# Optimization experiments

Measured on AMD Instinct MI355X. Metric: run time of the kernel, lower is better.

Reference implementation:

```python
import jax, jax.numpy as jnp
import numpy as np

EMB = 1024
HEADS = 16

def setup_inputs() -> dict:
    key = jax.random.key(0)
    ks = jax.random.split(key, 9)
    s = 1.0 / np.sqrt(EMB)
    x = jax.random.normal(ks[0], (2, 2048, EMB), dtype=jnp.float32)
    Wq = jax.random.normal(ks[1], (EMB, EMB), dtype=jnp.float32) * s
    bq = jax.random.normal(ks[2], (EMB,), dtype=jnp.float32) * s
    Wk = jax.random.normal(ks[3], (EMB, EMB), dtype=jnp.float32) * s
    bk = jax.random.normal(ks[4], (EMB,), dtype=jnp.float32) * s
    Wv = jax.random.normal(ks[5], (EMB, EMB), dtype=jnp.float32) * s
    bv = jax.random.normal(ks[6], (EMB,), dtype=jnp.float32) * s
    Wo = jax.random.normal(ks[7], (EMB, EMB), dtype=jnp.float32) * s
    bo = jax.random.normal(ks[8], (EMB,), dtype=jnp.float32) * s
    return {"x": x, "Wq": Wq, "bq": bq, "Wk": Wk, "bk": bk, "Wv": Wv, "bv": bv, "Wo": Wo, "bo": bo}

def reference(x, Wq, bq, Wk, bk, Wv, bv, Wo, bo):
    B, N, E = x.shape
    H = HEADS
    D = E // H
    # q/k/v projections, split heads: b n (h d) -> b h n d
    def proj(W, b):
        y = jnp.einsum('bne,ef->bnf', x, W.T) + b
        return y.reshape(B, N, H, D).transpose(0, 2, 1, 3)
    q = proj(Wq, bq)
    k = proj(Wk, bk)
    v = proj(Wv, bv)
    energy = jnp.einsum('bhqd,bhkd->bhqk', q, k)
    scaling = jnp.asarray(E, x.dtype) ** 0.5  # note: sqrt(emb_size), as in source
    att = jax.nn.softmax(energy / scaling, axis=-1)
    out = jnp.einsum('bhqk,bhkd->bhqd', att, v)
    out = out.transpose(0, 2, 1, 3).reshape(B, N, E)  # b h n d -> b n (h d)
    return jnp.einsum('bne,ef->bnf', out, Wo.T) + bo
```

## Files before the change

### kernel.cpp

```cpp
#include <hip/hip_runtime.h>
#include <hip/hip_bf16.h>
#include <stdint.h>

typedef __bf16 bf16;
typedef __bf16 bf16x8 __attribute__((ext_vector_type(8)));
typedef __bf16 bf16x4 __attribute__((ext_vector_type(4)));
typedef __bf16 bf16x2 __attribute__((ext_vector_type(2)));
typedef float  f32x4  __attribute__((ext_vector_type(4)));
typedef float  f32x16 __attribute__((ext_vector_type(16)));
typedef unsigned int uint;

#define MFMA(a,b,c)   __builtin_amdgcn_mfma_f32_16x16x32_bf16((a),(b),(c),0,0,0)
#define MFMA32(a,b,c) __builtin_amdgcn_mfma_f32_32x32x16_bf16((a),(b),(c),0,0,0)
#define EXP2(x)       __builtin_amdgcn_exp2f(x)

__device__ __forceinline__ void gload_lds16(const void* g, void* lds) {
  __builtin_amdgcn_global_load_lds(
      (const __attribute__((address_space(1))) uint32_t*)g,
      (__attribute__((address_space(3))) uint32_t*)lds, 16, 0, 0);
}

__device__ __forceinline__ uint pk_bf16(float lo, float hi) {
  bf16x2 v; v[0] = (bf16)lo; v[1] = (bf16)hi;
  return __builtin_bit_cast(uint, v);
}

__global__ __launch_bounds__(256) void k_cvt(
    const float* __restrict__ x,
    const float* __restrict__ wq, const float* __restrict__ wk,
    const float* __restrict__ wv, const float* __restrict__ wo,
    bf16* __restrict__ xb, bf16* __restrict__ wqb, bf16* __restrict__ wkb,
    bf16* __restrict__ wvb, bf16* __restrict__ wob)
{
  int r = blockIdx.y;
  const float* s; bf16* d; int n;
  switch (r) {
    case 0: s = x;  d = xb;  n = 4194304; break;
    case 1: s = wq; d = wqb; n = 1048576; break;
    case 2: s = wk; d = wkb; n = 1048576; break;
    case 3: s = wv; d = wvb; n = 1048576; break;
    default: s = wo; d = wob; n = 1048576; break;
  }
  int i = (blockIdx.x * 256 + threadIdx.x) * 8;
  if (i >= n) return;
  const float4* sp = (const float4*)(s + i);
  float4 a = sp[0], b = sp[1];
  bf16x8 o;
  o[0]=(bf16)a.x; o[1]=(bf16)a.y; o[2]=(bf16)a.z; o[3]=(bf16)a.w;
  o[4]=(bf16)b.x; o[5]=(bf16)b.y; o[6]=(bf16)b.z; o[7]=(bf16)b.w;
  *(bf16x8*)(d + i) = o;
}

__global__ __launch_bounds__(256, 2) void k_gemm_qkv(
    const bf16* __restrict__ A,
    const bf16* __restrict__ Wq, const bf16* __restrict__ Wk, const bf16* __restrict__ Wv,
    const float* __restrict__ bq, const float* __restrict__ bk, const float* __restrict__ bv,
    bf16* __restrict__ Qw, bf16* __restrict__ Kw, bf16* __restrict__ Vtw)
{
  __shared__ __align__(16) char As[2][8192];
  __shared__ __align__(16) char Bs[2][8192];
  int tid = threadIdx.x;
  int wv4 = tid >> 6, l = tid & 63, lo = l & 15, hi = l >> 4;
  int f = blockIdx.y * 32 + blockIdx.x;
  int xcd = f & 7, i8 = f >> 3;
  int mt = xcd * 4 + (i8 & 3);
  int ft = i8 >> 2;
  int wsel = ft >> 3;
  const bf16* W = (wsel == 0) ? Wq : (wsel == 1) ? Wk : Wv;
  const float* bias = (wsel == 0) ? bq : (wsel == 1) ? bk : bv;
  int f0 = (ft & 7) * 128;
  const bf16* Ab = A + (size_t)mt * 128 * 1024;
  const bf16* Wb = W + (size_t)f0 * 1024;
  const bf16* Pa = (wsel < 2) ? Wb : Ab;
  const bf16* Pb = (wsel < 2) ? Ab : Wb;
  int wm = wv4 >> 1, wf = wv4 & 1;
  f32x4 acc[4][4];
  #pragma unroll
  for (int i = 0; i < 4; i++)
    #pragma unroll
    for (int j = 0; j < 4; j++) acc[i][j] = (f32x4){0.f, 0.f, 0.f, 0.f};

  #define STAGEG(t, bi) {                                              \
    int k0 = (t) * 32;                                                 \
    _Pragma("unroll")                                                  \
    for (int p = 0; p < 2; p++) {                                      \
      int sp = p * 256 + tid;                                          \
      int row = sp >> 2, s = sp & 3;                                   \
      int gc = k0 + 8 * (s ^ ((row >> 1) & 3));                        \
      gload_lds16(Pa + (size_t)row * 1024 + gc, As[bi] + sp * 16);     \
      gload_lds16(Pb + (size_t)row * 1024 + gc, Bs[bi] + sp * 16);     \
    } }

  STAGEG(0, 0);
  for (int t = 0; t < 32; ++t) {
    __syncthreads();
    if (t < 31) STAGEG(t + 1, (t + 1) & 1);
    const char* Ac = As[t & 1];
    const char* Bc = Bs[t & 1];
    bf16x8 af[4], bfr[4];
    #pragma unroll
    for (int ms = 0; ms < 4; ms++) {
      int row = wm * 64 + ms * 16 + lo;
      af[ms] = *(const bf16x8*)(Ac + row * 64 + 16 * (hi ^ ((row >> 1) & 3)));
    }
    #pragma unroll
    for (int fs = 0; fs < 4; fs++) {
      int row = wf * 64 + fs * 16 + lo;
      bfr[fs] = *(const bf16x8*)(Bc + row * 64 + 16 * (hi ^ ((row >> 1) & 3)));
    }
    __builtin_amdgcn_s_setprio(1);
    #pragma unroll
    for (int ms = 0; ms < 4; ms++)
      #pragma unroll
      for (int fs = 0; fs < 4; fs++)
        acc[ms][fs] = MFMA(af[ms], bfr[fs], acc[ms][fs]);
    __builtin_amdgcn_s_setprio(0);
  }
  #undef STAGEG

  if (wsel < 2) {
    bf16* Outp = (wsel == 0) ? Qw : Kw;
    float qs = (wsel == 0) ? 0.0450842199527801f : 1.0f;
    #pragma unroll
    for (int ms = 0; ms < 4; ms++) {
      int fl = f0 + wm * 64 + ms * 16 + hi * 4;
      int h = fl >> 6, dd = fl & 63;
      float4 b4 = *(const float4*)(bias + fl);
      #pragma unroll
      for (int fs = 0; fs < 4; fs++) {
        int m = mt * 128 + wf * 64 + fs * 16 + lo;
        int b = m >> 11, nn = m & 2047;
        bf16x4 w;
        #pragma unroll
        for (int r = 0; r < 4; r++)
          w[r] = (bf16)((acc[ms][fs][r] + ((const float*)&b4)[r]) * qs);
        *(bf16x4*)(Outp + (((size_t)(b * 16 + h) * 2048 + nn) * 64) + dd) = w;
      }
    }
  } else {
    #pragma unroll
    for (int fs = 0; fs < 4; fs++) {
      int fl = f0 + wf * 64 + fs * 16 + lo;
      int h = fl >> 6, dd = fl & 63;
      float bb = bias[fl];
      #pragma unroll
      for (int ms = 0; ms < 4; ms++) {
        int m = mt * 128 + wm * 64 + ms * 16 + hi * 4;
        int b = m >> 11, nn = m & 2047;
        bf16x4 w;
        #pragma unroll
        for (int r = 0; r < 4; r++) w[r] = (bf16)(acc[ms][fs][r] + bb);
        *(bf16x4*)(Vtw + (((size_t)(b * 16 + h) * 64 + dd) * 2048) + nn) = w;
      }
    }
  }
}

__global__ __launch_bounds__(256, 2) void k_attn(
    const bf16* __restrict__ Q, const bf16* __restrict__ K,
    const bf16* __restrict__ Vt, bf16* __restrict__ O)
{
  __shared__ __align__(16) char Ks[2][8192];
  __shared__ __align__(16) char Vs[2][8192];
  int tid = threadIdx.x;
  int wid = tid >> 6, l = tid & 63;
  int lq = l & 31, hi1 = l >> 5;
  int f = blockIdx.y * 16 + blockIdx.x;
  int xcd = f & 7, i8 = f >> 3;
  int bh = xcd * 4 + (i8 & 3);
  int qt = i8 >> 2;
  int qg = qt * 128 + wid * 32 + lq;
  const bf16* Kb = K + (size_t)bh * 2048 * 64;
  const bf16* Vb = Vt + (size_t)bh * 64 * 2048;

  bf16x8 qf[4];
  const bf16* Qb = Q + ((size_t)bh * 2048 + qg) * 64 + hi1 * 8;
  #pragma unroll
  for (int c = 0; c < 4; c++) qf[c] = *(const bf16x8*)(Qb + 16 * c);

  f32x16 o0, o1, zz;
  #pragma unroll
  for (int r = 0; r < 16; r++) { zz[r] = 0.f; o0[r] = 0.f; o1[r] = 0.f; }
  float ls = 0.f;

  int srow = tid >> 3, slot = tid & 7;
  int swz = 16 * (slot ^ (srow & 7));
  int swk = lq & 7;
  uint4 k0r, k1r, v0r, v1r;
  #define STAGE(t) {                                                          \
    k0r = *(const uint4*)(Kb + (size_t)((t)*64 + srow) * 64 + slot * 8);      \
    k1r = *(const uint4*)(Kb + (size_t)((t)*64 + srow + 32) * 64 + slot * 8); \
    v0r = *(const uint4*)(Vb + (size_t)srow * 2048 + (t)*64 + slot * 8);      \
    v1r = *(const uint4*)(Vb + (size_t)(srow + 32) * 2048 + (t)*64 + slot * 8); }
  #define WRBUF(bi) {                                  \
    *(uint4*)(Ks[bi] + srow * 128 + swz)        = k0r; \
    *(uint4*)(Ks[bi] + (srow + 32) * 128 + swz) = k1r; \
    *(uint4*)(Vs[bi] + srow * 128 + swz)        = v0r; \
    *(uint4*)(Vs[bi] + (srow + 32) * 128 + swz) = v1r; }
  #define EXPSUM(S, T0, T1, T2, T3)                     \
    _Pragma("unroll")                                   \
    for (int r = 0; r < 16; r += 4) {                   \
      S[r]   = EXP2(S[r]);   T0 += S[r];                \
      S[r+1] = EXP2(S[r+1]); T1 += S[r+1];              \
      S[r+2] = EXP2(S[r+2]); T2 += S[r+2];              \
      S[r+3] = EXP2(S[r+3]); T3 += S[r+3];              \
    }
  #define PACK(dst, plo, phi)                                                \
    _Pragma("unroll")                                                        \
    for (int m = 0; m < 2; m++) {                                            \
      uint a0 = pk_bf16(plo[8*m+0], plo[8*m+1]);                             \
      uint b0 = pk_bf16(plo[8*m+4], plo[8*m+5]);                             \
      asm volatile("v_permlane32_swap_b32 %0, %1" : "+v"(a0), "+v"(b0));     \
      uint a1 = pk_bf16(plo[8*m+2], plo[8*m+3]);                             \
      uint b1 = pk_bf16(plo[8*m+6], plo[8*m+7]);                             \
      asm volatile("v_permlane32_swap_b32 %0, %1" : "+v"(a1), "+v"(b1));     \
      dst[m] = (uint4){a0, a1, b0, b1};                                      \
      uint c0 = pk_bf16(phi[8*m+0], phi[8*m+1]);                             \
      uint d0 = pk_bf16(phi[8*m+4], phi[8*m+5]);                             \
      asm volatile("v_permlane32_swap_b32 %0, %1" : "+v"(c0), "+v"(d0));     \
      uint c1 = pk_bf16(phi[8*m+2], phi[8*m+3]);                             \
      uint d1 = pk_bf16(phi[8*m+6], phi[8*m+7]);                             \
      asm volatile("v_permlane32_swap_b32 %0, %1" : "+v"(c1), "+v"(d1));     \
      dst[2+m] = (uint4){c0, c1, d0, d1};                                    \
    }

  STAGE(0);
  WRBUF(0);
  STAGE(1);

  for (int t = 0; t < 32; ++t) {
    __syncthreads();
    const char* Kc = Ks[t & 1];
    const char* Vc = Vs[t & 1];

    bf16x8 kf0[4], kf1[4];
    #pragma unroll
    for (int c = 0; c < 4; c++) {
      kf0[c] = *(const bf16x8*)(Kc + lq * 128 + 16 * ((2*c + hi1) ^ swk));
      kf1[c] = *(const bf16x8*)(Kc + (32 + lq) * 128 + 16 * ((2*c + hi1) ^ swk));
    }

    __builtin_amdgcn_s_setprio(1);
    f32x16 s0 = MFMA32(kf0[0], qf[0], zz);
    f32x16 s1 = MFMA32(kf1[0], qf[0], zz);
    #pragma unroll
    for (int c = 1; c < 4; c++) {
      s0 = MFMA32(kf0[c], qf[c], s0);
      s1 = MFMA32(kf1[c], qf[c], s1);
    }
    __builtin_amdgcn_s_setprio(0);

    float t0 = 0.f, t1 = 0.f, t2 = 0.f, t3 = 0.f;
    EXPSUM(s0, t0, t1, t2, t3);
    EXPSUM(s1, t0, t1, t2, t3);
    ls += (t0 + t1) + (t2 + t3);

    uint4 pf[4];
    PACK(pf, s0, s1);

    __builtin_amdgcn_s_setprio(1);
    #pragma unroll
    for (int c = 0; c < 4; c++) {
      bf16x8 pb = __builtin_bit_cast(bf16x8, pf[c]);
      bf16x8 vf0 = *(const bf16x8*)(Vc + lq * 128 + 16 * ((2*c + hi1) ^ swk));
      o0 = MFMA32(vf0, pb, o0);
      bf16x8 vf1 = *(const bf16x8*)(Vc + (32 + lq) * 128 + 16 * ((2*c + hi1) ^ swk));
      o1 = MFMA32(vf1, pb, o1);
    }
    __builtin_amdgcn_s_setprio(0);

    if (t < 31) {
      WRBUF((t + 1) & 1);
      if (t < 30) STAGE(t + 2);
    }
  }
  #undef STAGE
  #undef WRBUF

  float lsum = ls + __shfl_xor(ls, 32);
  float inv = 1.0f / lsum;
  int b = bh >> 4, h = bh & 15;
  bf16* Ob = O + ((size_t)(b * 2048 + qg)) * 1024 + h * 64 + hi1 * 4;
  #pragma unroll
  for (int g = 0; g < 4; g++) {
    bf16x4 w0, w1;
    #pragma unroll
    for (int j = 0; j < 4; j++) {
      w0[j] = (bf16)(o0[4*g+j] * inv);
      w1[j] = (bf16)(o1[4*g+j] * inv);
    }
    *(bf16x4*)(Ob + g * 8)      = w0;
    *(bf16x4*)(Ob + 32 + g * 8) = w1;
  }
}

__global__ __launch_bounds__(512, 1) void k_gemm_out(
    const bf16* __restrict__ A,
    const bf16* __restrict__ W,
    const float* __restrict__ bias,
    float* __restrict__ Cout)
{
  __shared__ __align__(16) char As[2][16384];
  __shared__ __align__(16) char Bs[2][16384];
  int tid = threadIdx.x;
  int wid = tid >> 6, l = tid & 63, lo = l & 15, hi = l >> 4;
  int f = blockIdx.y * 32 + blockIdx.x;
  int xcd = f & 7, i8 = f >> 3;
  int mt = xcd * 4 + (i8 & 3);
  int f0 = (i8 >> 2) * 128;
  const bf16* Ab = A + (size_t)mt * 128 * 1024;
  const bf16* Wb = W + (size_t)f0 * 1024;
  int wm2 = wid >> 2, wf4 = wid & 3;
  f32x4 acc[2][4];
  #pragma unroll
  for (int i = 0; i < 2; i++)
    #pragma unroll
    for (int j = 0; j < 4; j++) acc[i][j] = (f32x4){0.f, 0.f, 0.f, 0.f};

  #define STAGEG(t, bi) {                                              \
    int k0 = (t) * 64;                                                 \
    _Pragma("unroll")                                                  \
    for (int p = 0; p < 2; p++) {                                      \
      int sp = p * 512 + tid;                                          \
      int row = sp >> 3, s = sp & 7;                                   \
      int gc = k0 + 8 * (s ^ (row & 7));                               \
      gload_lds16(Wb + (size_t)row * 1024 + gc, As[bi] + sp * 16);     \
      gload_lds16(Ab + (size_t)row * 1024 + gc, Bs[bi] + sp * 16);     \
    } }

  STAGEG(0, 0);
  for (int t = 0; t < 16; ++t) {
    __syncthreads();
    if (t < 15) STAGEG(t + 1, (t + 1) & 1);
    const char* Ac = As[t & 1];
    const char* Bc = Bs[t & 1];
    #pragma unroll
    for (int kk = 0; kk < 2; kk++) {
      bf16x8 wfr[2], afr[4];
      #pragma unroll
      for (int i = 0; i < 2; i++) {
        int row = wf4 * 32 + i * 16 + lo;
        wfr[i] = *(const bf16x8*)(Ac + row * 128 + 16 * ((kk * 4 + hi) ^ (row & 7)));
      }
      #pragma unroll
      for (int j = 0; j < 4; j++) {
        int row = wm2 * 64 + j * 16 + lo;
        afr[j] = *(const bf16x8*)(Bc + row * 128 + 16 * ((kk * 4 + hi) ^ (row & 7)));
      }
      __builtin_amdgcn_s_setprio(1);
      #pragma unroll
      for (int i = 0; i < 2; i++)
        #pragma unroll
        for (int j = 0; j < 4; j++)
          acc[i][j] = MFMA(wfr[i], afr[j], acc[i][j]);
      __builtin_amdgcn_s_setprio(0);
    }
  }
  #undef STAGEG

  #pragma unroll
  for (int i = 0; i < 2; i++) {
    int fl = f0 + wf4 * 32 + i * 16 + hi * 4;
    float4 b4 = *(const float4*)(bias + fl);
    #pragma unroll
    for (int j = 0; j < 4; j++) {
      int m = mt * 128 + wm2 * 64 + j * 16 + lo;
      float4 o;
      o.x = acc[i][j][0] + b4.x;
      o.y = acc[i][j][1] + b4.y;
      o.z = acc[i][j][2] + b4.z;
      o.w = acc[i][j][3] + b4.w;
      *(float4*)(Cout + (size_t)m * 1024 + fl) = o;
    }
  }
}

extern "C" void kernel_launch(void* const* d_in, const int* in_sizes, int n_in,
                              void* d_out, int out_size, void* d_ws, size_t ws_size,
                              hipStream_t stream) {
  const float* x  = (const float*)d_in[0];
  const float* Wq = (const float*)d_in[1];
  const float* bq = (const float*)d_in[2];
  const float* Wk = (const float*)d_in[3];
  const float* bk = (const float*)d_in[4];
  const float* Wv = (const float*)d_in[5];
  const float* bv = (const float*)d_in[6];
  const float* Wo = (const float*)d_in[7];
  const float* bo = (const float*)d_in[8];
  float* out = (float*)d_out;
  char* ws = (char*)d_ws;

  bf16* xb  = (bf16*)(ws);
  bf16* wqb = (bf16*)(ws + 8388608);
  bf16* wkb = (bf16*)(ws + 10485760);
  bf16* wvb = (bf16*)(ws + 12582912);
  bf16* wob = (bf16*)(ws + 14680064);
  bf16* Qw  = (bf16*)(ws + 16777216);
  bf16* Kw  = (bf16*)(ws + 25165824);
  bf16* Vtw = (bf16*)(ws + 33554432);
  bf16* Ow  = (bf16*)(ws + 41943040);

  k_cvt<<<dim3(2048, 5), 256, 0, stream>>>(x, Wq, Wk, Wv, Wo, xb, wqb, wkb, wvb, wob);
  k_gemm_qkv<<<dim3(32, 24), 256, 0, stream>>>(xb, wqb, wkb, wvb, bq, bk, bv, Qw, Kw, Vtw);
  k_attn<<<dim3(16, 32), 256, 0, stream>>>(Qw, Kw, Vtw, Ow);
  k_gemm_out<<<dim3(32, 8), 512, 0, stream>>>(Ow, wob, bo, out);
}
```

Before: 106.1 us.

## Process two 64-key sub-tiles per iteration with interleaved QK, softmax and PV

After: 113.1 us. +6.6%, slower.

```diff
diff --git a/kernel.cpp b/kernel.cpp
--- a/kernel.cpp
+++ b/kernel.cpp
@@ -160,8 +160,8 @@
     const bf16* __restrict__ Q, const bf16* __restrict__ K,
     const bf16* __restrict__ Vt, bf16* __restrict__ O)
 {
-  __shared__ __align__(16) char Ks[2][8192];
-  __shared__ __align__(16) char Vs[2][8192];
+  __shared__ __align__(16) char Ks[2][16384];
+  __shared__ __align__(16) char Vs[2][16384];
   int tid = threadIdx.x;
   int wid = tid >> 6, l = tid & 63;
   int lq = l & 31, hi1 = l >> 5;
@@ -178,25 +178,33 @@
   #pragma unroll
   for (int c = 0; c < 4; c++) qf[c] = *(const bf16x8*)(Qb + 16 * c);
 
-  f32x16 o0, o1, zz;
-  #pragma unroll
-  for (int r = 0; r < 16; r++) { zz[r] = 0.f; o0[r] = 0.f; o1[r] = 0.f; }
+  f32x16 oA0, oA1, oB0, oB1, zz;
+  #pragma unroll
+  for (int r = 0; r < 16; r++) { zz[r] = 0.f; oA0[r] = 0.f; oA1[r] = 0.f; oB0[r] = 0.f; oB1[r] = 0.f; }
   float ls = 0.f;
 
   int srow = tid >> 3, slot = tid & 7;
   int swz = 16 * (slot ^ (srow & 7));
   int swk = lq & 7;
-  uint4 k0r, k1r, v0r, v1r;
-  #define STAGE(t) {                                                          \
-    k0r = *(const uint4*)(Kb + (size_t)((t)*64 + srow) * 64 + slot * 8);      \
-    k1r = *(const uint4*)(Kb + (size_t)((t)*64 + srow + 32) * 64 + slot * 8); \
-    v0r = *(const uint4*)(Vb + (size_t)srow * 2048 + (t)*64 + slot * 8);      \
-    v1r = *(const uint4*)(Vb + (size_t)(srow + 32) * 2048 + (t)*64 + slot * 8); }
-  #define WRBUF(bi) {                                  \
-    *(uint4*)(Ks[bi] + srow * 128 + swz)        = k0r; \
-    *(uint4*)(Ks[bi] + (srow + 32) * 128 + swz) = k1r; \
-    *(uint4*)(Vs[bi] + srow * 128 + swz)        = v0r; \
-    *(uint4*)(Vs[bi] + (srow + 32) * 128 + swz) = v1r; }
+  uint4 k0r, k1r, k2r, k3r, v0r, v1r, v2r, v3r;
+  #define STAGE(t) {                                                               \
+    k0r = *(const uint4*)(Kb + (size_t)((t)*128 + srow) * 64 + slot * 8);          \
+    k1r = *(const uint4*)(Kb + (size_t)((t)*128 + srow + 32) * 64 + slot * 8);     \
+    k2r = *(const uint4*)(Kb + (size_t)((t)*128 + srow + 64) * 64 + slot * 8);     \
+    k3r = *(const uint4*)(Kb + (size_t)((t)*128 + srow + 96) * 64 + slot * 8);     \
+    v0r = *(const uint4*)(Vb + (size_t)srow * 2048 + (t)*128 + slot * 8);          \
+    v1r = *(const uint4*)(Vb + (size_t)(srow + 32) * 2048 + (t)*128 + slot * 8);   \
+    v2r = *(const uint4*)(Vb + (size_t)srow * 2048 + (t)*128 + 64 + slot * 8);     \
+    v3r = *(const uint4*)(Vb + (size_t)(srow + 32) * 2048 + (t)*128 + 64 + slot * 8); }
+  #define WRBUF(bi) {                                          \
+    *(uint4*)(Ks[bi] + srow * 128 + swz)             = k0r;    \
+    *(uint4*)(Ks[bi] + (srow + 32) * 128 + swz)      = k1r;    \
+    *(uint4*)(Ks[bi] + (srow + 64) * 128 + swz)      = k2r;    \
+    *(uint4*)(Ks[bi] + (srow + 96) * 128 + swz)      = k3r;    \
+    *(uint4*)(Vs[bi] + srow * 128 + swz)             = v0r;    \
+    *(uint4*)(Vs[bi] + (srow + 32) * 128 + swz)      = v1r;    \
+    *(uint4*)(Vs[bi] + 8192 + srow * 128 + swz)      = v2r;    \
+    *(uint4*)(Vs[bi] + 8192 + (srow + 32) * 128 + swz) = v3r; }
   #define EXPSUM(S, T0, T1, T2, T3)                     \
     _Pragma("unroll")                                   \
     for (int r = 0; r < 16; r += 4) {                   \
@@ -228,55 +236,96 @@
   WRBUF(0);
   STAGE(1);
 
-  for (int t = 0; t < 32; ++t) {
+  for (int t = 0; t < 16; ++t) {
     __syncthreads();
     const char* Kc = Ks[t & 1];
     const char* Vc = Vs[t & 1];
 
-    bf16x8 kf0[4], kf1[4];
+    bf16x8 ka0[4], ka1[4];
     #pragma unroll
     for (int c = 0; c < 4; c++) {
-      kf0[c] = *(const bf16x8*)(Kc + lq * 128 + 16 * ((2*c + hi1) ^ swk));
-      kf1[c] = *(const bf16x8*)(Kc + (32 + lq) * 128 + 16 * ((2*c + hi1) ^ swk));
-    }
-
+      ka0[c] = *(const bf16x8*)(Kc + lq * 128 + 16 * ((2*c + hi1) ^ swk));
+      ka1[c] = *(const bf16x8*)(Kc + (32 + lq) * 128 + 16 * ((2*c + hi1) ^ swk));
+    }
     __builtin_amdgcn_s_setprio(1);
-    f32x16 s0 = MFMA32(kf0[0], qf[0], zz);
-    f32x16 s1 = MFMA32(kf1[0], qf[0], zz);
+    f32x16 sA0 = MFMA32(ka0[0], qf[0], zz);
+    f32x16 sA1 = MFMA32(ka1[0], qf[0], zz);
     #pragma unroll
     for (int c = 1; c < 4; c++) {
-      s0 = MFMA32(kf0[c], qf[c], s0);
-      s1 = MFMA32(kf1[c], qf[c], s1);
+      sA0 = MFMA32(ka0[c], qf[c], sA0);
+      sA1 = MFMA32(ka1[c], qf[c], sA1);
     }
     __builtin_amdgcn_s_setprio(0);
 
-    float t0 = 0.f, t1 = 0.f, t2 = 0.f, t3 = 0.f;
-    EXPSUM(s0, t0, t1, t2, t3);
-    EXPSUM(s1, t0, t1, t2, t3);
-    ls += (t0 + t1) + (t2 + t3);
-
-    uint4 pf[4];
-    PACK(pf, s0, s1);
+    bf16x8 kb0[4], kb1[4];
+    #pragma unroll
+    for (int c = 0; c < 4; c++) {
+      kb0[c] = *(const bf16x8*)(Kc + 8192 + lq * 128 + 16 * ((2*c + hi1) ^ swk));
+      kb1[c] = *(const bf16x8*)(Kc + 8192 + (32 + lq) * 128 + 16 * ((2*c + hi1) ^ swk));
+    }
+
+    float a0 = 0.f, a1 = 0.f, a2 = 0.f, a3 = 0.f;
+    EXPSUM(sA0, a0, a1, a2, a3);
+    EXPSUM(sA1, a0, a1, a2, a3);
 
     __builtin_amdgcn_s_setprio(1);
+    f32x16 sB0 = MFMA32(kb0[0], qf[0], zz);
+    f32x16 sB1 = MFMA32(kb1[0], qf[0], zz);
+    #pragma unroll
+    for (int c = 1; c < 4; c++) {
+      sB0 = MFMA32(kb0[c], qf[c], sB0);
+      sB1 = MFMA32(kb1[c], qf[c], sB1);
+    }
+    __builtin_amdgcn_s_setprio(0);
+
+    uint4 pfA[4];
+    PACK(pfA, sA0, sA1);
+
+    bf16x8 va0[4], va1[4];
     #pragma unroll
     for (int c = 0; c < 4; c++) {
-      bf16x8 pb = __builtin_bit_cast(bf16x8, pf[c]);
-      bf16x8 vf0 = *(const bf16x8*)(Vc + lq * 128 + 16 * ((2*c + hi1) ^ swk));
-      o0 = MFMA32(vf0, pb, o0);
-      bf16x8 vf1 = *(const bf16x8*)(Vc + (32 + lq) * 128 + 16 * ((2*c + hi1) ^ swk));
-      o1 = MFMA32(vf1, pb, o1);
+      va0[c] = *(const bf16x8*)(Vc + lq * 128 + 16 * ((2*c + hi1) ^ swk));
+      va1[c] = *(const bf16x8*)(Vc + (32 + lq) * 128 + 16 * ((2*c + hi1) ^ swk));
+    }
+
+    float b0 = 0.f, b1 = 0.f, b2 = 0.f, b3 = 0.f;
+    EXPSUM(sB0, b0, b1, b2, b3);
+    EXPSUM(sB1, b0, b1, b2, b3);
+    ls += ((a0 + a1) + (a2 + a3)) + ((b0 + b1) + (b2 + b3));
+
+    __builtin_amdgcn_s_setprio(1);
+    #pragma unroll
+    for (int c = 0; c < 4; c++) {
+      bf16x8 pb = __builtin_bit_cast(bf16x8, pfA[c]);
+      oA0 = MFMA32(va0[c], pb, oA0);
+      oA1 = MFMA32(va1[c], pb, oA1);
     }
     __builtin_amdgcn_s_setprio(0);
 
-    if (t < 31) {
+    uint4 pfB[4];
+    PACK(pfB, sB0, sB1);
+
+    __builtin_amdgcn_s_setprio(1);
+    #pragma unroll
+    for (int c = 0; c < 4; c++) {
+      bf16x8 pb = __builtin_bit_cast(bf16x8, pfB[c]);
+      bf16x8 vb0 = *(const bf16x8*)(Vc + 8192 + lq * 128 + 16 * ((2*c + hi1) ^ swk));
+      oB0 = MFMA32(vb0, pb, oB0);
+      bf16x8 vb1 = *(const bf16x8*)(Vc + 8192 + (32 + lq) * 128 + 16 * ((2*c + hi1) ^ swk));
+      oB1 = MFMA32(vb1, pb, oB1);
+    }
+    __builtin_amdgcn_s_setprio(0);
+
+    if (t < 15) {
       WRBUF((t + 1) & 1);
-      if (t < 30) STAGE(t + 2);
+      if (t < 14) STAGE(t + 2);
     }
   }
   #undef STAGE
   #undef WRBUF
 
+  f32x16 o0 = oA0 + oB0;
+  f32x16 o1 = oA1 + oB1;
   float lsum = ls + __shfl_xor(ls, 32);
   float inv = 1.0f / lsum;
   int b = bh >> 4, h = bh & 15;
```

## Software-pipeline attention loop with triple-buffered LDS and QK^T lookahead

Applied to the files above, without the earlier changes.

Measured after the change: 108.8 us. +2.5%, slower.

```diff
diff --git a/kernel.cpp b/kernel.cpp
--- a/kernel.cpp
+++ b/kernel.cpp
@@ -160,8 +160,8 @@
     const bf16* __restrict__ Q, const bf16* __restrict__ K,
     const bf16* __restrict__ Vt, bf16* __restrict__ O)
 {
-  __shared__ __align__(16) char Ks[2][8192];
-  __shared__ __align__(16) char Vs[2][8192];
+  __shared__ __align__(16) char Ks[3][8192];
+  __shared__ __align__(16) char Vs[3][8192];
   int tid = threadIdx.x;
   int wid = tid >> 6, l = tid & 63;
   int lq = l & 31, hi1 = l >> 5;
@@ -223,59 +223,61 @@
       asm volatile("v_permlane32_swap_b32 %0, %1" : "+v"(c1), "+v"(d1));     \
       dst[2+m] = (uint4){c0, c1, d0, d1};                                    \
     }
-
-  STAGE(0);
-  WRBUF(0);
-  STAGE(1);
-
-  for (int t = 0; t < 32; ++t) {
-    __syncthreads();
-    const char* Kc = Ks[t & 1];
-    const char* Vc = Vs[t & 1];
-
-    bf16x8 kf0[4], kf1[4];
-    #pragma unroll
-    for (int c = 0; c < 4; c++) {
-      kf0[c] = *(const bf16x8*)(Kc + lq * 128 + 16 * ((2*c + hi1) ^ swk));
-      kf1[c] = *(const bf16x8*)(Kc + (32 + lq) * 128 + 16 * ((2*c + hi1) ^ swk));
-    }
-
-    __builtin_amdgcn_s_setprio(1);
-    f32x16 s0 = MFMA32(kf0[0], qf[0], zz);
-    f32x16 s1 = MFMA32(kf1[0], qf[0], zz);
-    #pragma unroll
-    for (int c = 1; c < 4; c++) {
-      s0 = MFMA32(kf0[c], qf[c], s0);
-      s1 = MFMA32(kf1[c], qf[c], s1);
-    }
-    __builtin_amdgcn_s_setprio(0);
-
-    float t0 = 0.f, t1 = 0.f, t2 = 0.f, t3 = 0.f;
-    EXPSUM(s0, t0, t1, t2, t3);
-    EXPSUM(s1, t0, t1, t2, t3);
-    ls += (t0 + t1) + (t2 + t3);
-
-    uint4 pf[4];
-    PACK(pf, s0, s1);
-
-    __builtin_amdgcn_s_setprio(1);
-    #pragma unroll
-    for (int c = 0; c < 4; c++) {
-      bf16x8 pb = __builtin_bit_cast(bf16x8, pf[c]);
-      bf16x8 vf0 = *(const bf16x8*)(Vc + lq * 128 + 16 * ((2*c + hi1) ^ swk));
-      o0 = MFMA32(vf0, pb, o0);
-      bf16x8 vf1 = *(const bf16x8*)(Vc + (32 + lq) * 128 + 16 * ((2*c + hi1) ^ swk));
-      o1 = MFMA32(vf1, pb, o1);
-    }
-    __builtin_amdgcn_s_setprio(0);
-
-    if (t < 31) {
-      WRBUF((t + 1) & 1);
-      if (t < 30) STAGE(t + 2);
-    }
+  #define QKT(bi, S0, S1) {                                                  \
+    bf16x8 kf0[4], kf1[4];                                                   \
+    _Pragma("unroll")                                                        \
+    for (int c = 0; c < 4; c++) {                                            \
+      kf0[c] = *(const bf16x8*)(Ks[bi] + lq * 128 + 16 * ((2*c + hi1) ^ swk));        \
+      kf1[c] = *(const bf16x8*)(Ks[bi] + (32 + lq) * 128 + 16 * ((2*c + hi1) ^ swk)); \
+    }                                                                        \
+    __builtin_amdgcn_s_setprio(1);                                           \
+    S0 = MFMA32(kf0[0], qf[0], zz);                                          \
+    S1 = MFMA32(kf1[0], qf[0], zz);                                          \
+    _Pragma("unroll")                                                        \
+    for (int c = 1; c < 4; c++) {                                            \
+      S0 = MFMA32(kf0[c], qf[c], S0);                                        \
+      S1 = MFMA32(kf1[c], qf[c], S1);                                        \
+    }                                                                        \
+    __builtin_amdgcn_s_setprio(0); }
+  #define SMPV(bi, S0, S1) {                                                 \
+    float e0 = 0.f, e1 = 0.f, e2 = 0.f, e3 = 0.f;                            \
+    EXPSUM(S0, e0, e1, e2, e3);                                              \
+    EXPSUM(S1, e0, e1, e2, e3);                                              \
+    ls += (e0 + e1) + (e2 + e3);                                             \
+    uint4 pf[4];                                                             \
+    PACK(pf, S0, S1);                                                        \
+    __builtin_amdgcn_s_setprio(1);                                           \
+    _Pragma("unroll")                                                        \
+    for (int c = 0; c < 4; c++) {                                            \
+      bf16x8 pb = __builtin_bit_cast(bf16x8, pf[c]);                         \
+      bf16x8 vf0 = *(const bf16x8*)(Vs[bi] + lq * 128 + 16 * ((2*c + hi1) ^ swk));        \
+      o0 = MFMA32(vf0, pb, o0);                                              \
+      bf16x8 vf1 = *(const bf16x8*)(Vs[bi] + (32 + lq) * 128 + 16 * ((2*c + hi1) ^ swk)); \
+      o1 = MFMA32(vf1, pb, o1);                                              \
+    }                                                                        \
+    __builtin_amdgcn_s_setprio(0); }
+  #define BODY(t, SC0, SC1, SN0, SN1) {                                      \
+    __syncthreads();                                                         \
+    if ((t) < 31) QKT(((t) + 1) % 3, SN0, SN1);                              \
+    if ((t) < 30) WRBUF(((t) + 2) % 3);                                      \
+    SMPV((t) % 3, SC0, SC1);                                                 \
+    if ((t) < 29) STAGE((t) + 3); }
+
+  STAGE(0); WRBUF(0); STAGE(1);
+  __syncthreads();
+  WRBUF(1); STAGE(2);
+  f32x16 sA0, sA1, sB0, sB1;
+  QKT(0, sA0, sA1);
+
+  for (int tt = 0; tt < 32; tt += 2) {
+    BODY(tt,     sA0, sA1, sB0, sB1);
+    BODY(tt + 1, sB0, sB1, sA0, sA1);
   }
   #undef STAGE
   #undef WRBUF
+  #undef QKT
+  #undef SMPV
+  #undef BODY
 
   float lsum = ls + __shfl_xor(ls, 32);
   float inv = 1.0f / lsum;
```

## Split attention KV loop across wave pairs, each wave handling 64 queries

Applied to the files above, without the earlier changes.

Result: no change. 104.4 us (-1.6%).

```diff
diff --git a/kernel.cpp b/kernel.cpp
--- a/kernel.cpp
+++ b/kernel.cpp
@@ -160,43 +160,58 @@
     const bf16* __restrict__ Q, const bf16* __restrict__ K,
     const bf16* __restrict__ Vt, bf16* __restrict__ O)
 {
-  __shared__ __align__(16) char Ks[2][8192];
-  __shared__ __align__(16) char Vs[2][8192];
+  __shared__ __align__(16) char Ks[4][8192];
+  __shared__ __align__(16) char Vs[4][8192];
   int tid = threadIdx.x;
   int wid = tid >> 6, l = tid & 63;
   int lq = l & 31, hi1 = l >> 5;
+  int qhalf = wid >> 1, kpar = wid & 1;
   int f = blockIdx.y * 16 + blockIdx.x;
   int xcd = f & 7, i8 = f >> 3;
   int bh = xcd * 4 + (i8 & 3);
   int qt = i8 >> 2;
-  int qg = qt * 128 + wid * 32 + lq;
+  int q0 = qt * 128 + qhalf * 64;
   const bf16* Kb = K + (size_t)bh * 2048 * 64;
   const bf16* Vb = Vt + (size_t)bh * 64 * 2048;
 
-  bf16x8 qf[4];
-  const bf16* Qb = Q + ((size_t)bh * 2048 + qg) * 64 + hi1 * 8;
+  bf16x8 qf0[4], qf1[4];
+  const bf16* Qb = Q + ((size_t)bh * 2048 + q0) * 64 + hi1 * 8;
   #pragma unroll
-  for (int c = 0; c < 4; c++) qf[c] = *(const bf16x8*)(Qb + 16 * c);
-
-  f32x16 o0, o1, zz;
+  for (int c = 0; c < 4; c++) {
+    qf0[c] = *(const bf16x8*)(Qb + (size_t)lq * 64 + 16 * c);
+    qf1[c] = *(const bf16x8*)(Qb + (size_t)(lq + 32) * 64 + 16 * c);
+  }
+
+  f32x16 o00, o01, o10, o11, zz;
   #pragma unroll
-  for (int r = 0; r < 16; r++) { zz[r] = 0.f; o0[r] = 0.f; o1[r] = 0.f; }
-  float ls = 0.f;
+  for (int r = 0; r < 16; r++) { zz[r] = 0.f; o00[r] = 0.f; o01[r] = 0.f; o10[r] = 0.f; o11[r] = 0.f; }
+  float ls0 = 0.f, ls1 = 0.f;
 
   int srow = tid >> 3, slot = tid & 7;
   int swz = 16 * (slot ^ (srow & 7));
   int swk = lq & 7;
-  uint4 k0r, k1r, v0r, v1r;
-  #define STAGE(t) {                                                          \
-    k0r = *(const uint4*)(Kb + (size_t)((t)*64 + srow) * 64 + slot * 8);      \
-    k1r = *(const uint4*)(Kb + (size_t)((t)*64 + srow + 32) * 64 + slot * 8); \
-    v0r = *(const uint4*)(Vb + (size_t)srow * 2048 + (t)*64 + slot * 8);      \
-    v1r = *(const uint4*)(Vb + (size_t)(srow + 32) * 2048 + (t)*64 + slot * 8); }
-  #define WRBUF(bi) {                                  \
-    *(uint4*)(Ks[bi] + srow * 128 + swz)        = k0r; \
-    *(uint4*)(Ks[bi] + (srow + 32) * 128 + swz) = k1r; \
-    *(uint4*)(Vs[bi] + srow * 128 + swz)        = v0r; \
-    *(uint4*)(Vs[bi] + (srow + 32) * 128 + swz) = v1r; }
+  uint4 xk0, xk1, xv0, xv1;
+  uint4 yk0, yk1, yv0, yv1;
+  #define STAGEX(t) {                                                          \
+    xk0 = *(const uint4*)(Kb + (size_t)((t)*64 + srow) * 64 + slot * 8);       \
+    xk1 = *(const uint4*)(Kb + (size_t)((t)*64 + srow + 32) * 64 + slot * 8);  \
+    xv0 = *(const uint4*)(Vb + (size_t)srow * 2048 + (t)*64 + slot * 8);       \
+    xv1 = *(const uint4*)(Vb + (size_t)(srow + 32) * 2048 + (t)*64 + slot * 8); }
+  #define STAGEY(t) {                                                          \
+    yk0 = *(const uint4*)(Kb + (size_t)((t)*64 + srow) * 64 + slot * 8);       \
+    yk1 = *(const uint4*)(Kb + (size_t)((t)*64 + srow + 32) * 64 + slot * 8);  \
+    yv0 = *(const uint4*)(Vb + (size_t)srow * 2048 + (t)*64 + slot * 8);       \
+    yv1 = *(const uint4*)(Vb + (size_t)(srow + 32) * 2048 + (t)*64 + slot * 8); }
+  #define WRX(bi) {                                     \
+    *(uint4*)(Ks[bi] + srow * 128 + swz)        = xk0;  \
+    *(uint4*)(Ks[bi] + (srow + 32) * 128 + swz) = xk1;  \
+    *(uint4*)(Vs[bi] + srow * 128 + swz)        = xv0;  \
+    *(uint4*)(Vs[bi] + (srow + 32) * 128 + swz) = xv1; }
+  #define WRY(bi) {                                     \
+    *(uint4*)(Ks[bi] + srow * 128 + swz)        = yk0;  \
+    *(uint4*)(Ks[bi] + (srow + 32) * 128 + swz) = yk1;  \
+    *(uint4*)(Vs[bi] + srow * 128 + swz)        = yv0;  \
+    *(uint4*)(Vs[bi] + (srow + 32) * 128 + swz) = yv1; }
   #define EXPSUM(S, T0, T1, T2, T3)                     \
     _Pragma("unroll")                                   \
     for (int r = 0; r < 16; r += 4) {                   \
@@ -224,14 +239,19 @@
       dst[2+m] = (uint4){c0, c1, d0, d1};                                    \
     }
 
-  STAGE(0);
-  WRBUF(0);
-  STAGE(1);
-
-  for (int t = 0; t < 32; ++t) {
+  STAGEX(0); STAGEY(1);
+  WRX(0); WRY(2);
+  STAGEX(2); STAGEY(3);
+
+  for (int e = 0; e < 16; ++e) {
     __syncthreads();
-    const char* Kc = Ks[t & 1];
-    const char* Vc = Vs[t & 1];
+    if (e < 15) {
+      WRX((e + 1) & 1);
+      WRY(2 + ((e + 1) & 1));
+    }
+    int bi = kpar ? (2 + (e & 1)) : (e & 1);
+    const char* Kc = (const char*)Ks + (size_t)bi * 8192;
+    const char* Vc = (const char*)Vs + (size_t)bi * 8192;
 
     bf16x8 kf0[4], kf1[4];
     #pragma unroll
@@ -239,58 +259,104 @@
       kf0[c] = *(const bf16x8*)(Kc + lq * 128 + 16 * ((2*c + hi1) ^ swk));
       kf1[c] = *(const bf16x8*)(Kc + (32 + lq) * 128 + 16 * ((2*c + hi1) ^ swk));
     }
-
     __builtin_amdgcn_s_setprio(1);
-    f32x16 s0 = MFMA32(kf0[0], qf[0], zz);
-    f32x16 s1 = MFMA32(kf1[0], qf[0], zz);
+    f32x16 s00 = MFMA32(kf0[0], qf0[0], zz);
+    f32x16 s01 = MFMA32(kf1[0], qf0[0], zz);
+    f32x16 s10 = MFMA32(kf0[0], qf1[0], zz);
+    f32x16 s11 = MFMA32(kf1[0], qf1[0], zz);
     #pragma unroll
     for (int c = 1; c < 4; c++) {
-      s0 = MFMA32(kf0[c], qf[c], s0);
-      s1 = MFMA32(kf1[c], qf[c], s1);
+      s00 = MFMA32(kf0[c], qf0[c], s00);
+      s01 = MFMA32(kf1[c], qf0[c], s01);
+      s10 = MFMA32(kf0[c], qf1[c], s10);
+      s11 = MFMA32(kf1[c], qf1[c], s11);
     }
     __builtin_amdgcn_s_setprio(0);
 
     float t0 = 0.f, t1 = 0.f, t2 = 0.f, t3 = 0.f;
-    EXPSUM(s0, t0, t1, t2, t3);
-    EXPSUM(s1, t0, t1, t2, t3);
-    ls += (t0 + t1) + (t2 + t3);
-
-    uint4 pf[4];
-    PACK(pf, s0, s1);
+    float u0 = 0.f, u1 = 0.f, u2 = 0.f, u3 = 0.f;
+    EXPSUM(s00, t0, t1, t2, t3);
+    EXPSUM(s01, t0, t1, t2, t3);
+    EXPSUM(s10, u0, u1, u2, u3);
+    EXPSUM(s11, u0, u1, u2, u3);
+    ls0 += (t0 + t1) + (t2 + t3);
+    ls1 += (u0 + u1) + (u2 + u3);
+
+    uint4 pf0[4], pf1[4];
+    PACK(pf0, s00, s01);
+    PACK(pf1, s10, s11);
 
     __builtin_amdgcn_s_setprio(1);
     #pragma unroll
     for (int c = 0; c < 4; c++) {
-      bf16x8 pb = __builtin_bit_cast(bf16x8, pf[c]);
       bf16x8 vf0 = *(const bf16x8*)(Vc + lq * 128 + 16 * ((2*c + hi1) ^ swk));
-      o0 = MFMA32(vf0, pb, o0);
       bf16x8 vf1 = *(const bf16x8*)(Vc + (32 + lq) * 128 + 16 * ((2*c + hi1) ^ swk));
-      o1 = MFMA32(vf1, pb, o1);
+      bf16x8 p0b = __builtin_bit_cast(bf16x8, pf0[c]);
+      bf16x8 p1b = __builtin_bit_cast(bf16x8, pf1[c]);
+      o00 = MFMA32(vf0, p0b, o00);
+      o01 = MFMA32(vf1, p0b, o01);
+      o10 = MFMA32(vf0, p1b, o10);
+      o11 = MFMA32(vf1, p1b, o11);
     }
     __builtin_amdgcn_s_setprio(0);
 
-    if (t < 31) {
-      WRBUF((t + 1) & 1);
-      if (t < 30) STAGE(t + 2);
-    }
-  }
-  #undef STAGE
-  #undef WRBUF
-
-  float lsum = ls + __shfl_xor(ls, 32);
-  float inv = 1.0f / lsum;
-  int b = bh >> 4, h = bh & 15;
-  bf16* Ob = O + ((size_t)(b * 2048 + qg)) * 1024 + h * 64 + hi1 * 4;
-  #pragma unroll
-  for (int g = 0; g < 4; g++) {
-    bf16x4 w0, w1;
-    #pragma unroll
-    for (int j = 0; j < 4; j++) {
-      w0[j] = (bf16)(o0[4*g+j] * inv);
-      w1[j] = (bf16)(o1[4*g+j] * inv);
-    }
-    *(bf16x4*)(Ob + g * 8)      = w0;
-    *(bf16x4*)(Ob + 32 + g * 8) = w1;
+    if (e < 14) { STAGEX(2 * e + 4); STAGEY(2 * e + 5); }
+  }
+  #undef STAGEX
+  #undef STAGEY
+  #undef WRX
+  #undef WRY
+
+  __syncthreads();
+  float* sc = (float*)(qhalf ? (char*)Vs : (char*)Ks) + 68 * l;
+  if (kpar == 1) {
+    #pragma unroll
+    for (int g = 0; g < 4; g++) {
+      *(f32x4*)(sc + 4*g)      = (f32x4){o00[4*g], o00[4*g+1], o00[4*g+2], o00[4*g+3]};
+      *(f32x4*)(sc + 16 + 4*g) = (f32x4){o01[4*g], o01[4*g+1], o01[4*g+2], o01[4*g+3]};
+      *(f32x4*)(sc + 32 + 4*g) = (f32x4){o10[4*g], o10[4*g+1], o10[4*g+2], o10[4*g+3]};
+      *(f32x4*)(sc + 48 + 4*g) = (f32x4){o11[4*g], o11[4*g+1], o11[4*g+2], o11[4*g+3]};
+    }
+    sc[64] = ls0; sc[65] = ls1;
+  }
+  __syncthreads();
+  if (kpar == 0) {
+    #pragma unroll
+    for (int g = 0; g < 4; g++) {
+      f32x4 a0 = *(const f32x4*)(sc + 4*g);
+      f32x4 a1 = *(const f32x4*)(sc + 16 + 4*g);
+      f32x4 a2 = *(const f32x4*)(sc + 32 + 4*g);
+      f32x4 a3 = *(const f32x4*)(sc + 48 + 4*g);
+      #pragma unroll
+      for (int j = 0; j < 4; j++) {
+        o00[4*g+j] += a0[j];
+        o01[4*g+j] += a1[j];
+        o10[4*g+j] += a2[j];
+        o11[4*g+j] += a3[j];
+      }
+    }
+    ls0 += sc[64]; ls1 += sc[65];
+    float lA = ls0 + __shfl_xor(ls0, 32);
+    float lB = ls1 + __shfl_xor(ls1, 32);
+    float inv0 = 1.0f / lA, inv1 = 1.0f / lB;
+    int b = bh >> 4, h = bh & 15;
+    bf16* Ob0 = O + ((size_t)(b * 2048 + q0 + lq)) * 1024 + h * 64 + hi1 * 4;
+    bf16* Ob1 = O + ((size_t)(b * 2048 + q0 + 32 + lq)) * 1024 + h * 64 + hi1 * 4;
+    #pragma unroll
+    for (int g = 0; g < 4; g++) {
+      bf16x4 w0, w1, w2, w3;
+      #pragma unroll
+      for (int j = 0; j < 4; j++) {
+        w0[j] = (bf16)(o00[4*g+j] * inv0);
+        w1[j] = (bf16)(o01[4*g+j] * inv0);
+        w2[j] = (bf16)(o10[4*g+j] * inv1);
+        w3[j] = (bf16)(o11[4*g+j] * inv1);
+      }
+      *(bf16x4*)(Ob0 + g * 8)      = w0;
+      *(bf16x4*)(Ob0 + 32 + g * 8) = w1;
+      *(bf16x4*)(Ob1 + g * 8)      = w2;
+      *(bf16x4*)(Ob1 + 32 + g * 8) = w3;
+    }
   }
 }
 
```
